# Performance work log

Hardware: AMD Instinct MI355X
Metric: run time of the kernel (lower is better)

## Reference

```python
import jax, jax.numpy as jnp
import numpy as np

TG22 = 0.4142135623730951  # tan(22.5 deg)
TG67 = 2.414213562373095   # tan(67.5 deg)


def _canny(gray):
    # gray: [B,H,W] float in [0,255]; cv2 path casts to uint8 -> truncate
    g = jnp.floor(jnp.clip(gray, 0.0, 255.0))
    p = jnp.pad(g, ((0, 0), (1, 1), (1, 1)), mode='edge')  # BORDER_REPLICATE
    # Sobel 3x3 (cross-correlation) via shifted slices
    gx = (p[:, :-2, 2:] + 2.0 * p[:, 1:-1, 2:] + p[:, 2:, 2:]
          - p[:, :-2, :-2] - 2.0 * p[:, 1:-1, :-2] - p[:, 2:, :-2])
    gy = (p[:, 2:, :-2] + 2.0 * p[:, 2:, 1:-1] + p[:, 2:, 2:]
          - p[:, :-2, :-2] - 2.0 * p[:, :-2, 1:-1] - p[:, :-2, 2:])
    mag = jnp.abs(gx) + jnp.abs(gy)  # cv2.Canny default L1 gradient
    # 8 neighbors of magnitude (zero-padded)
    pm = jnp.pad(mag, ((0, 0), (1, 1), (1, 1)))
    e = pm[:, 1:-1, 2:]; w = pm[:, 1:-1, :-2]
    n = pm[:, :-2, 1:-1]; s = pm[:, 2:, 1:-1]
    nw = pm[:, :-2, :-2]; se = pm[:, 2:, 2:]
    ne = pm[:, :-2, 2:]; sw = pm[:, 2:, :-2]
    # quantize gradient direction into 4 bins and do non-max suppression
    ax, ay = jnp.abs(gx), jnp.abs(gy)
    horiz = ay <= TG22 * ax          # gradient ~horizontal -> compare E/W
    vert = ay > TG67 * ax            # gradient ~vertical   -> compare N/S
    same_sign = (gx * gy) >= 0.0     # 45-deg diagonal choice
    n1 = jnp.where(horiz, e, jnp.where(vert, n, jnp.where(same_sign, nw, ne)))
    n2 = jnp.where(horiz, w, jnp.where(vert, s, jnp.where(same_sign, se, sw)))
    keep = (mag > n1) & (mag >= n2)
    nms = jnp.where(keep, mag, 0.0)
    strong = nms > 150.0
    weak = nms > 50.0

    def dilate3x3(m):
        mp = jnp.pad(m, ((0, 0), (1, 1), (1, 1)))
        H, W_ = m.shape[1], m.shape[2]
        acc = m
        for di in (0, 1, 2):
            for dj in (0, 1, 2):
                acc = acc | mp[:, di:di + H, dj:dj + W_]
        return acc

    # hysteresis: grow strong into connected weak pixels until fixed point
    def cond(st):
        prev, cur = st
        return jnp.any(prev != cur)

    def body(st):
        _, cur = st
        nxt = cur | (weak & dilate3x3(cur))
        return (cur, nxt)

    _, final = jax.lax.while_loop(cond, body, (jnp.zeros_like(strong), strong))
    return final.astype(jnp.float32) * 255.0  # cv2.Canny outputs 0/255


def setup_inputs() -> dict:
    key = jax.random.key(0)
    k1, k2, k3 = jax.random.split(key, 3)
    B, C, H, W_ = 16, 3, 512, 512
    OC = 32
    x = jax.random.uniform(k1, (B, C, H, W_), dtype=jnp.float32) * 255.0
    W = jax.random.normal(k2, (OC, C + 1), dtype=jnp.float32) * (1.0 / np.sqrt(C + 1))
    b = jax.random.normal(k3, (OC,), dtype=jnp.float32) * 0.01
    return {"x": x, "W": W, "b": b}


def reference(x, W, b):
    # grayscale
    gray = 0.2989 * x[:, 0] + 0.587 * x[:, 1] + 0.114 * x[:, 2]  # [B,H,W]
    # edge branch is detached in the original (cpu().detach())
    edge = jax.lax.stop_gradient(_canny(gray))[:, None]  # [B,1,H,W]
    cat = jnp.concatenate([x, edge], axis=1)  # [B,4,H,W]
    out = jnp.einsum('bchw,oc->bohw', cat, W) + b[None, :, None, None]
    return jax.nn.relu(out)
```

## Files before the change

kernel.cpp:

```cpp
#include <hip/hip_runtime.h>
#include <stdint.h>

typedef unsigned long long u64;

#define MD_OFF   (4ull << 20)
#define WK_OFF   (12ull << 20)
#define ST_OFF   ((12ull << 20) + (512ull << 10))
#define ED_OFF   ((12ull << 20) + (1024ull << 10))

__global__ __launch_bounds__(256) void k_gray(const float* __restrict__ x,
                                              unsigned char* __restrict__ g) {
#pragma clang fp contract(off)
    const float C0 = (float)0.2989, C1 = (float)0.587, C2 = (float)0.114;
    int i   = blockIdx.x * 256 + threadIdx.x;
    int b   = i >> 16;
    int rem = i & 65535;
    const float* xb = x + (size_t)b * 786432 + (size_t)rem * 4;
    float4 r0 = *(const float4*)(xb);
    float4 r1 = *(const float4*)(xb + 262144);
    float4 r2 = *(const float4*)(xb + 524288);
    float g0 = C0 * r0.x + C1 * r1.x + C2 * r2.x;
    float g1 = C0 * r0.y + C1 * r1.y + C2 * r2.y;
    float g2 = C0 * r0.z + C1 * r1.z + C2 * r2.z;
    float g3 = C0 * r0.w + C1 * r1.w + C2 * r2.w;
    g0 = floorf(fminf(fmaxf(g0, 0.0f), 255.0f));
    g1 = floorf(fminf(fmaxf(g1, 0.0f), 255.0f));
    g2 = floorf(fminf(fmaxf(g2, 0.0f), 255.0f));
    g3 = floorf(fminf(fmaxf(g3, 0.0f), 255.0f));
    uchar4 st = make_uchar4((unsigned char)g0, (unsigned char)g1,
                            (unsigned char)g2, (unsigned char)g3);
    *(uchar4*)(g + (size_t)b * 262144 + (size_t)rem * 4) = st;
}

__global__ __launch_bounds__(256) void k_sobel(const unsigned char* __restrict__ g,
                                               unsigned short* __restrict__ magdir) {
    const float TG22f = (float)0.4142135623730951;
    const float TG67f = (float)2.414213562373095;
    int i = blockIdx.x * 256 + threadIdx.x;
    int b = i >> 18;
    int r = (i >> 9) & 511;
    int w = i & 511;
    const unsigned char* gb = g + (size_t)b * 262144;
    int rm = r > 0 ? r - 1 : 0, rp = r < 511 ? r + 1 : 511;
    int wm = w > 0 ? w - 1 : 0, wp = w < 511 ? w + 1 : 511;
    int a00 = gb[rm * 512 + wm], a01 = gb[rm * 512 + w], a02 = gb[rm * 512 + wp];
    int a10 = gb[r  * 512 + wm],                          a12 = gb[r  * 512 + wp];
    int a20 = gb[rp * 512 + wm], a21 = gb[rp * 512 + w],  a22 = gb[rp * 512 + wp];
    int gx = a02 + 2 * a12 + a22 - a00 - 2 * a10 - a20;
    int gy = a20 + 2 * a21 + a22 - a00 - 2 * a01 - a02;
    int ax = gx < 0 ? -gx : gx;
    int ay = gy < 0 ? -gy : gy;
    int mag = ax + ay;
    float fax = (float)ax, fay = (float)ay;
    unsigned dir;
    if (fay <= TG22f * fax)      dir = 0u;
    else if (fay > TG67f * fax)  dir = 1u;
    else                         dir = (gx * gy >= 0) ? 2u : 3u;
    magdir[i] = (unsigned short)(mag | (dir << 12));
}

__global__ __launch_bounds__(256) void k_nms(const unsigned short* __restrict__ magdir,
                                             u64* __restrict__ weakw,
                                             u64* __restrict__ strongw) {
    int i = blockIdx.x * 256 + threadIdx.x;
    int b = i >> 18;
    int r = (i >> 9) & 511;
    int w = i & 511;
    const unsigned short* mb = magdir + (size_t)b * 262144;
    int md  = mb[r * 512 + w];
    int mag = md & 0x7FF;
    int dir = md >> 12;
    auto ldm = [&](int rr, int ww) -> int {
        if ((unsigned)rr > 511u || (unsigned)ww > 511u) return 0;
        return (int)(mb[rr * 512 + ww] & 0x7FF);
    };
    int n1, n2;
    if (dir == 0)      { n1 = ldm(r, w + 1);     n2 = ldm(r, w - 1); }
    else if (dir == 1) { n1 = ldm(r - 1, w);     n2 = ldm(r + 1, w); }
    else if (dir == 2) { n1 = ldm(r - 1, w - 1); n2 = ldm(r + 1, w + 1); }
    else               { n1 = ldm(r - 1, w + 1); n2 = ldm(r + 1, w - 1); }
    bool keep = (mag > n1) && (mag >= n2);
    int nms = keep ? mag : 0;
    u64 wb = __ballot(nms > 50);
    u64 sb = __ballot(nms > 150);
    int widx = ((b << 9) + r) * 8 + (w >> 6);
    int lane = threadIdx.x & 63;
    if (lane == 0) weakw[widx]   = wb;
    else if (lane == 1) strongw[widx] = sb;
}

__device__ inline u64 upfill(u64 w, u64 s) {
    return ((((w + s) ^ w) & w) | s);
}
__device__ inline u64 runfill(u64 w, u64 s) {
    u64 u = upfill(w, s);
    u64 d = __brevll(upfill(__brevll(w), __brevll(s)));
    return u | d;
}

__global__ __launch_bounds__(512) void k_hyst(const u64* __restrict__ weakg,
                                              const u64* __restrict__ strongg,
                                              u64* __restrict__ edgeg) {
    __shared__ u64 cur[4096];
    __shared__ int sflag;
    int b = blockIdx.x;
    int t = threadIdx.x;
    const u64* wk = weakg + (size_t)b * 4096;
    const u64* st = strongg + (size_t)b * 4096;
    int c  = t & 7;
    int r0 = (t >> 3) * 8;
    u64 wreg[8];
#pragma unroll
    for (int j = 0; j < 8; ++j) {
        int idx = (r0 + j) * 8 + c;
        wreg[j] = wk[idx];
        cur[idx] = st[idx];
    }
    __syncthreads();

    for (int it = 0;; ++it) {
        if (t == 0) sflag = 0;
        __syncthreads();
        bool ch = false;
        bool down = (it & 1) == 0;
        u64 carry = 0;
        for (int k = 0; k < 8; ++k) {
            int j = down ? k : 7 - k;
            int r = r0 + j;
            int idx = r * 8 + c;
            u64 wv = wreg[j];
            u64 self = cur[idx];
            if (self == wv) { carry = self; continue; }
            u64 um = (r > 0)   ? ((down && k > 0)  ? carry : cur[idx - 8]) : 0;
            u64 dm = (r < 511) ? ((!down && k > 0) ? carry : cur[idx + 8]) : 0;
            u64 lor = 0, ror_ = 0;
            if (c > 0) {
                u64 lm = cur[idx - 1];
                u64 lu = (r > 0)   ? cur[idx - 9] : 0;
                u64 ld = (r < 511) ? cur[idx + 7] : 0;
                lor = lm | lu | ld;
            }
            if (c < 7) {
                u64 rm = cur[idx + 1];
                u64 ru = (r > 0)   ? cur[idx - 7] : 0;
                u64 rd = (r < 511) ? cur[idx + 9] : 0;
                ror_ = rm | ru | rd;
            }
            u64 vert = um | dm | self;
            u64 dil = vert | (vert << 1) | (vert >> 1) | (lor >> 63) | (ror_ << 63);
            u64 nv = self | (wv & dil);
            nv = runfill(wv, nv);
            carry = nv;
            if (nv != self) { cur[idx] = nv; ch = true; }
        }
        if (ch) sflag = 1;
        __syncthreads();
        if (!sflag) break;
        __syncthreads();
    }

    u64* eg = edgeg + (size_t)b * 4096;
#pragma unroll
    for (int j = 0; j < 8; ++j) {
        int idx = (r0 + j) * 8 + c;
        eg[idx] = cur[idx];
    }
}

__global__ __launch_bounds__(256) void k_out(const float* __restrict__ x,
                                             const float* __restrict__ Wm,
                                             const float* __restrict__ bv,
                                             const u64* __restrict__ edgeg,
                                             float* __restrict__ out) {
    __shared__ float sW[128];
    __shared__ float sb[32];
    if (threadIdx.x < 128) sW[threadIdx.x] = Wm[threadIdx.x];
    if (threadIdx.x < 32)  sb[threadIdx.x] = bv[threadIdx.x];
    __syncthreads();
    int i   = blockIdx.x * 256 + threadIdx.x;
    int b   = i >> 16;
    int rem = i & 65535;
    size_t pix = (size_t)rem * 4;
    const float* xb = x + (size_t)b * 786432;
    float4 x0 = *(const float4*)(xb + pix);
    float4 x1 = *(const float4*)(xb + 262144 + pix);
    float4 x2 = *(const float4*)(xb + 524288 + pix);
    int r  = rem >> 7;
    int wq = rem & 127;
    u64 ew = edgeg[(((size_t)b * 512 + r) * 8) + (wq >> 4)];
    int sh = (wq & 15) * 4;
    float e0 = ((ew >> (sh + 0)) & 1ull) ? 255.0f : 0.0f;
    float e1 = ((ew >> (sh + 1)) & 1ull) ? 255.0f : 0.0f;
    float e2 = ((ew >> (sh + 2)) & 1ull) ? 255.0f : 0.0f;
    float e3 = ((ew >> (sh + 3)) & 1ull) ? 255.0f : 0.0f;
    float* ob = out + (size_t)b * 32 * 262144 + pix;
#pragma unroll 4
    for (int o = 0; o < 32; ++o) {
        float w0 = sW[o * 4 + 0], w1 = sW[o * 4 + 1];
        float w2 = sW[o * 4 + 2], w3 = sW[o * 4 + 3];
        float bb = sb[o];
        float4 v;
        v.x = fmaxf(w0 * x0.x + w1 * x1.x + w2 * x2.x + w3 * e0 + bb, 0.0f);
        v.y = fmaxf(w0 * x0.y + w1 * x1.y + w2 * x2.y + w3 * e1 + bb, 0.0f);
        v.z = fmaxf(w0 * x0.z + w1 * x1.z + w2 * x2.z + w3 * e2 + bb, 0.0f);
        v.w = fmaxf(w0 * x0.w + w1 * x1.w + w2 * x2.w + w3 * e3 + bb, 0.0f);
        *(float4*)(ob + (size_t)o * 262144) = v;
    }
}

extern "C" void kernel_launch(void* const* d_in, const int* in_sizes, int n_in,
                              void* d_out, int out_size, void* d_ws, size_t ws_size,
                              hipStream_t stream) {
    const float* x  = (const float*)d_in[0];
    const float* Wm = (const float*)d_in[1];
    const float* bv = (const float*)d_in[2];
    float* out = (float*)d_out;
    char* ws = (char*)d_ws;

    unsigned char*  g      = (unsigned char*)(ws);
    unsigned short* magdir = (unsigned short*)(ws + MD_OFF);
    u64* weakw   = (u64*)(ws + WK_OFF);
    u64* strongw = (u64*)(ws + ST_OFF);
    u64* edgew   = (u64*)(ws + ED_OFF);

    k_gray<<<4096, 256, 0, stream>>>(x, g);
    k_sobel<<<16384, 256, 0, stream>>>(g, magdir);
    k_nms<<<16384, 256, 0, stream>>>(magdir, weakw, strongw);
    k_hyst<<<16, 512, 0, stream>>>(weakw, strongw, edgew);
    k_out<<<4096, 256, 0, stream>>>(x, Wm, bv, edgew, out);
}
```

Before: 683.8 us.

## Restructure hysteresis into single-wavefront bands with shuffle-based horizontal propagation

Hysteresis now runs one 64-thread wavefront per image instead of 512 threads. Each lane owns a 64-row band of one word column and sweeps it down and then up, carrying the just-updated row forward. Horizontal propagation between neighbouring word columns uses shuffles, iterated to closure within each row, so every barrier and shared-flag round is replaced by wavefront ballots. The intent is to spread connectivity much further per outer iteration and drop __syncthreads overhead, at the cost of far less parallelism per block and a serial 64-row dependency chain per lane.

```diff
diff --git a/kernel.cpp b/kernel.cpp
--- a/kernel.cpp
+++ b/kernel.cpp
@@ -98,72 +98,84 @@
     return u | d;
 }
 
-__global__ __launch_bounds__(512) void k_hyst(const u64* __restrict__ weakg,
-                                              const u64* __restrict__ strongg,
-                                              u64* __restrict__ edgeg) {
-    __shared__ u64 cur[4096];
-    __shared__ int sflag;
+__global__ __launch_bounds__(64) void k_hyst(const u64* __restrict__ weakg,
+                                             const u64* __restrict__ strongg,
+                                             u64* __restrict__ edgeg) {
+    __shared__ u64 sw[4096];
+    __shared__ u64 sc[4096];
     int b = blockIdx.x;
     int t = threadIdx.x;
     const u64* wk = weakg + (size_t)b * 4096;
     const u64* st = strongg + (size_t)b * 4096;
-    int c  = t & 7;
-    int r0 = (t >> 3) * 8;
-    u64 wreg[8];
-#pragma unroll
-    for (int j = 0; j < 8; ++j) {
-        int idx = (r0 + j) * 8 + c;
-        wreg[j] = wk[idx];
-        cur[idx] = st[idx];
-    }
-    __syncthreads();
-
-    for (int it = 0;; ++it) {
-        if (t == 0) sflag = 0;
-        __syncthreads();
+#pragma unroll 4
+    for (int i = 0; i < 64; ++i) {
+        int idx = i * 64 + t;
+        sw[idx] = wk[idx];
+        sc[idx] = st[idx];
+    }
+    int col  = t & 7;
+    int band = t >> 3;
+    int rbase = band * 64;
+    const bool hasL = col > 0, hasR = col < 7;
+
+    auto rowstep = [&](u64 w, u64 self, u64 carry, u64 other) -> u64 {
+        u64 vert = carry | other;
+        u64 lv = __shfl(vert, t - 1);
+        u64 rv = __shfl(vert, t + 1);
+        u64 dil = vert | (vert << 1) | (vert >> 1)
+                | (hasL ? (lv >> 63) : 0) | (hasR ? (rv << 63) : 0);
+        u64 nv = runfill(w, self | (w & dil));
+        for (;;) {
+            u64 ln = __shfl(nv, t - 1);
+            u64 rn = __shfl(nv, t + 1);
+            u64 hc = (hasL ? (ln >> 63) : 0) | (hasR ? (rn << 63) : 0);
+            u64 add = w & hc & ~nv;
+            if (__ballot(add != 0) == 0) break;
+            nv = runfill(w, nv | add);
+        }
+        return nv;
+    };
+
+    for (;;) {
         bool ch = false;
-        bool down = (it & 1) == 0;
-        u64 carry = 0;
-        for (int k = 0; k < 8; ++k) {
-            int j = down ? k : 7 - k;
-            int r = r0 + j;
-            int idx = r * 8 + c;
-            u64 wv = wreg[j];
-            u64 self = cur[idx];
-            if (self == wv) { carry = self; continue; }
-            u64 um = (r > 0)   ? ((down && k > 0)  ? carry : cur[idx - 8]) : 0;
-            u64 dm = (r < 511) ? ((!down && k > 0) ? carry : cur[idx + 8]) : 0;
-            u64 lor = 0, ror_ = 0;
-            if (c > 0) {
-                u64 lm = cur[idx - 1];
-                u64 lu = (r > 0)   ? cur[idx - 9] : 0;
-                u64 ld = (r < 511) ? cur[idx + 7] : 0;
-                lor = lm | lu | ld;
+        {
+            u64 carry = (rbase > 0) ? sc[(rbase - 1) * 8 + col] : 0;
+            u64 self  = sc[rbase * 8 + col];
+#pragma unroll 2
+            for (int k = 0; k < 64; ++k) {
+                int r = rbase + k;
+                int idx = r * 8 + col;
+                u64 w  = sw[idx];
+                u64 dn = (r < 511) ? sc[idx + 8] : 0;
+                u64 nv = rowstep(w, self, carry, dn);
+                if (nv != self) { sc[idx] = nv; ch = true; }
+                carry = nv;
+                self  = dn;
             }
-            if (c < 7) {
-                u64 rm = cur[idx + 1];
-                u64 ru = (r > 0)   ? cur[idx - 7] : 0;
-                u64 rd = (r < 511) ? cur[idx + 9] : 0;
-                ror_ = rm | ru | rd;
+        }
+        {
+            u64 carry = (rbase + 64 < 512) ? sc[(rbase + 64) * 8 + col] : 0;
+            u64 self  = sc[(rbase + 63) * 8 + col];
+#pragma unroll 2
+            for (int k = 63; k >= 0; --k) {
+                int r = rbase + k;
+                int idx = r * 8 + col;
+                u64 w  = sw[idx];
+                u64 up = (r > 0) ? sc[idx - 8] : 0;
+                u64 nv = rowstep(w, self, carry, up);
+                if (nv != self) { sc[idx] = nv; ch = true; }
+                carry = nv;
+                self  = up;
             }
-            u64 vert = um | dm | self;
-            u64 dil = vert | (vert << 1) | (vert >> 1) | (lor >> 63) | (ror_ << 63);
-            u64 nv = self | (wv & dil);
-            nv = runfill(wv, nv);
-            carry = nv;
-            if (nv != self) { cur[idx] = nv; ch = true; }
         }
-        if (ch) sflag = 1;
-        __syncthreads();
-        if (!sflag) break;
-        __syncthreads();
+        if (__ballot(ch) == 0) break;
     }
 
     u64* eg = edgeg + (size_t)b * 4096;
-#pragma unroll
-    for (int j = 0; j < 8; ++j) {
-        int idx = (r0 + j) * 8 + c;
-        eg[idx] = cur[idx];
+#pragma unroll 4
+    for (int i = 0; i < 64; ++i) {
+        int idx = i * 64 + t;
+        eg[idx] = sc[idx];
     }
 }
 
@@ -226,6 +238,6 @@
     k_gray<<<4096, 256, 0, stream>>>(x, g);
     k_sobel<<<16384, 256, 0, stream>>>(g, magdir);
     k_nms<<<16384, 256, 0, stream>>>(magdir, weakw, strongw);
-    k_hyst<<<16, 512, 0, stream>>>(weakw, strongw, edgew);
+    k_hyst<<<16, 64, 0, stream>>>(weakw, strongw, edgew);
     k_out<<<4096, 256, 0, stream>>>(x, Wm, bv, edgew, out);
 }
```

Measured after the change: 741.1 us. 1.08x slower.

## Double hysteresis threads, pad shared rows, sweep both directions per iteration

Applied to the files above, without the earlier changes.

The hysteresis kernel now runs 1024 threads per image, each owning 4 rows instead of 8. Each iteration does a downward sweep followed by an upward sweep. The shared bitmap rows are padded to stride 9 to avoid bank conflicts. The flag reset is also reorganized. Separately, the output kernel uses nontemporal vector stores and a larger unroll to reduce cache pollution from the large output write. Shorter per-thread chains may need more outer iterations to propagate edges, each with block-wide barriers.

```diff
diff --git a/kernel.cpp b/kernel.cpp
--- a/kernel.cpp
+++ b/kernel.cpp
@@ -2,6 +2,7 @@
 #include <stdint.h>
 
 typedef unsigned long long u64;
+typedef float __attribute__((ext_vector_type(4))) fvec4;
 
 #define MD_OFF   (4ull << 20)
 #define WK_OFF   (12ull << 20)
@@ -98,72 +99,111 @@
     return u | d;
 }
 
-__global__ __launch_bounds__(512) void k_hyst(const u64* __restrict__ weakg,
-                                              const u64* __restrict__ strongg,
-                                              u64* __restrict__ edgeg) {
-    __shared__ u64 cur[4096];
+#define HST 9
+
+__global__ __launch_bounds__(1024) void k_hyst(const u64* __restrict__ weakg,
+                                               const u64* __restrict__ strongg,
+                                               u64* __restrict__ edgeg) {
+    __shared__ u64 sc[512 * HST];
     __shared__ int sflag;
     int b = blockIdx.x;
     int t = threadIdx.x;
     const u64* wk = weakg + (size_t)b * 4096;
     const u64* st = strongg + (size_t)b * 4096;
+#pragma unroll
+    for (int i = 0; i < 4; ++i) {
+        int ig = i * 1024 + t;
+        int r = ig >> 3, c = ig & 7;
+        sc[r * HST + c] = st[ig];
+    }
     int c  = t & 7;
-    int r0 = (t >> 3) * 8;
-    u64 wreg[8];
-#pragma unroll
-    for (int j = 0; j < 8; ++j) {
-        int idx = (r0 + j) * 8 + c;
-        wreg[j] = wk[idx];
-        cur[idx] = st[idx];
-    }
+    int r0 = (t >> 3) * 4;
+    u64 wreg[4];
+#pragma unroll
+    for (int j = 0; j < 4; ++j) wreg[j] = wk[(r0 + j) * 8 + c];
+    if (t == 0) sflag = 0;
+    const bool hasL = c > 0, hasR = c < 7;
     __syncthreads();
 
-    for (int it = 0;; ++it) {
-        if (t == 0) sflag = 0;
-        __syncthreads();
+    for (;;) {
         bool ch = false;
-        bool down = (it & 1) == 0;
-        u64 carry = 0;
-        for (int k = 0; k < 8; ++k) {
-            int j = down ? k : 7 - k;
-            int r = r0 + j;
-            int idx = r * 8 + c;
-            u64 wv = wreg[j];
-            u64 self = cur[idx];
-            if (self == wv) { carry = self; continue; }
-            u64 um = (r > 0)   ? ((down && k > 0)  ? carry : cur[idx - 8]) : 0;
-            u64 dm = (r < 511) ? ((!down && k > 0) ? carry : cur[idx + 8]) : 0;
-            u64 lor = 0, ror_ = 0;
-            if (c > 0) {
-                u64 lm = cur[idx - 1];
-                u64 lu = (r > 0)   ? cur[idx - 9] : 0;
-                u64 ld = (r < 511) ? cur[idx + 7] : 0;
-                lor = lm | lu | ld;
+        {
+            u64 carry = (r0 > 0) ? sc[(r0 - 1) * HST + c] : 0;
+#pragma unroll
+            for (int j = 0; j < 4; ++j) {
+                int r = r0 + j;
+                int idx = r * HST + c;
+                u64 wv = wreg[j];
+                u64 self = sc[idx];
+                if (self == wv) { carry = self; continue; }
+                u64 dm = (r < 511) ? sc[idx + HST] : 0;
+                u64 lor = 0, ror_ = 0;
+                if (hasL) {
+                    u64 lm = sc[idx - 1];
+                    u64 lu = (r > 0)   ? sc[idx - HST - 1] : 0;
+                    u64 ld = (r < 511) ? sc[idx + HST - 1] : 0;
+                    lor = lm | lu | ld;
+                }
+                if (hasR) {
+                    u64 rm = sc[idx + 1];
+                    u64 ru = (r > 0)   ? sc[idx - HST + 1] : 0;
+                    u64 rd = (r < 511) ? sc[idx + HST + 1] : 0;
+                    ror_ = rm | ru | rd;
+                }
+                u64 vert = carry | dm | self;
+                u64 dil = vert | (vert << 1) | (vert >> 1)
+                        | (lor >> 63) | (ror_ << 63);
+                u64 nv = runfill(wv, self | (wv & dil));
+                if (nv != self) { sc[idx] = nv; ch = true; }
+                carry = nv;
             }
-            if (c < 7) {
-                u64 rm = cur[idx + 1];
-                u64 ru = (r > 0)   ? cur[idx - 7] : 0;
-                u64 rd = (r < 511) ? cur[idx + 9] : 0;
-                ror_ = rm | ru | rd;
+        }
+        {
+            u64 carry = (r0 + 4 < 512) ? sc[(r0 + 4) * HST + c] : 0;
+#pragma unroll
+            for (int j = 3; j >= 0; --j) {
+                int r = r0 + j;
+                int idx = r * HST + c;
+                u64 wv = wreg[j];
+                u64 self = sc[idx];
+                if (self == wv) { carry = self; continue; }
+                u64 um = (r > 0) ? sc[idx - HST] : 0;
+                u64 lor = 0, ror_ = 0;
+                if (hasL) {
+                    u64 lm = sc[idx - 1];
+                    u64 lu = (r > 0)   ? sc[idx - HST - 1] : 0;
+                    u64 ld = (r < 511) ? sc[idx + HST - 1] : 0;
+                    lor = lm | lu | ld;
+                }
+                if (hasR) {
+                    u64 rm = sc[idx + 1];
+                    u64 ru = (r > 0)   ? sc[idx - HST + 1] : 0;
+                    u64 rd = (r < 511) ? sc[idx + HST + 1] : 0;
+                    ror_ = rm | ru | rd;
+                }
+                u64 vert = um | carry | self;
+                u64 dil = vert | (vert << 1) | (vert >> 1)
+                        | (lor >> 63) | (ror_ << 63);
+                u64 nv = runfill(wv, self | (wv & dil));
+                if (nv != self) { sc[idx] = nv; ch = true; }
+                carry = nv;
             }
-            u64 vert = um | dm | self;
-            u64 dil = vert | (vert << 1) | (vert >> 1) | (lor >> 63) | (ror_ << 63);
-            u64 nv = self | (wv & dil);
-            nv = runfill(wv, nv);
-            carry = nv;
-            if (nv != self) { cur[idx] = nv; ch = true; }
         }
         if (ch) sflag = 1;
         __syncthreads();
-        if (!sflag) break;
+        bool stop = (sflag == 0);
         __syncthreads();
+        if (stop) break;
+        if (t == 0) sflag = 0;
+        __syncthreads();
     }
 
     u64* eg = edgeg + (size_t)b * 4096;
 #pragma unroll
-    for (int j = 0; j < 8; ++j) {
-        int idx = (r0 + j) * 8 + c;
-        eg[idx] = cur[idx];
+    for (int i = 0; i < 4; ++i) {
+        int ig = i * 1024 + t;
+        int r = ig >> 3, cc = ig & 7;
+        eg[ig] = sc[r * HST + cc];
     }
 }
 
@@ -194,17 +234,17 @@
     float e2 = ((ew >> (sh + 2)) & 1ull) ? 255.0f : 0.0f;
     float e3 = ((ew >> (sh + 3)) & 1ull) ? 255.0f : 0.0f;
     float* ob = out + (size_t)b * 32 * 262144 + pix;
-#pragma unroll 4
+#pragma unroll 8
     for (int o = 0; o < 32; ++o) {
         float w0 = sW[o * 4 + 0], w1 = sW[o * 4 + 1];
         float w2 = sW[o * 4 + 2], w3 = sW[o * 4 + 3];
         float bb = sb[o];
-        float4 v;
+        fvec4 v;
         v.x = fmaxf(w0 * x0.x + w1 * x1.x + w2 * x2.x + w3 * e0 + bb, 0.0f);
         v.y = fmaxf(w0 * x0.y + w1 * x1.y + w2 * x2.y + w3 * e1 + bb, 0.0f);
         v.z = fmaxf(w0 * x0.z + w1 * x1.z + w2 * x2.z + w3 * e2 + bb, 0.0f);
         v.w = fmaxf(w0 * x0.w + w1 * x1.w + w2 * x2.w + w3 * e3 + bb, 0.0f);
-        *(float4*)(ob + (size_t)o * 262144) = v;
+        __builtin_nontemporal_store(v, (fvec4*)(ob + (size_t)o * 262144));
     }
 }
 
@@ -226,6 +266,6 @@
     k_gray<<<4096, 256, 0, stream>>>(x, g);
     k_sobel<<<16384, 256, 0, stream>>>(g, magdir);
     k_nms<<<16384, 256, 0, stream>>>(magdir, weakw, strongw);
-    k_hyst<<<16, 512, 0, stream>>>(weakw, strongw, edgew);
+    k_hyst<<<16, 1024, 0, stream>>>(weakw, strongw, edgew);
     k_out<<<4096, 256, 0, stream>>>(x, Wm, bv, edgew, out);
 }
```

New measurement: 596.3 us. 12.8% less time.
